# Kernel optimization log

Hardware: AMD Instinct MI355X
Metric: run time of the kernel (lower is better)

## Reference

```python
import jax, jax.numpy as jnp
import numpy as np
from jax import lax

RES = 100      # resolution (default)
BETA = 0.1     # smooth_clamp beta

def smooth_clamp(x, lo, hi):
    return lo + (hi - lo) * jax.nn.sigmoid(BETA * (x - (lo + hi) / 2))

def setup_inputs() -> dict:
    R, C, TQ, TN = 4096, 2048, 4096, 4096
    key = jax.random.key(0)
    k1, k2, k3, k4 = jax.random.split(key, 4)
    t_init = jnp.linspace(0.0, 10.0, TN).astype(jnp.float32)
    t = jnp.sort(jax.random.uniform(k1, (TQ,), jnp.float32, 0.0, 10.0))
    init_conc = jax.random.uniform(k2, (C,), jnp.float32, 0.05, 1.0)
    # sparse stoichiometry: per reaction 2 reactants (-1) and 2 products (+1), distinct compounds
    rng = np.random.default_rng(0)
    idx = np.argsort(rng.random((R, C)), axis=1)[:, :4]
    nu_np = np.zeros((R, C), np.float32)
    nu_np[np.arange(R)[:, None], idx] = np.array([-1.0, -1.0, 1.0, 1.0], np.float32)
    nu = jnp.asarray(nu_np)
    # replicate torch __init__ order/ub math to pick sane raw params f, r
    stoi_f = jnp.where(nu < 0, 0.0, nu)
    stoi_r = jnp.where(nu > 0, 0.0, nu)
    order = jnp.stack([stoi_f.sum(1), -stoi_r.sum(1)], axis=1)          # (R,2)
    ub = TN * 10.0 / jnp.max(jnp.diff(t_init)) / init_conc.sum() ** (order - 1.0)
    kf = jax.random.uniform(k3, (R,), jnp.float32, 0.05, 0.5)
    kr = jax.random.uniform(k4, (R,), jnp.float32, 0.05, 0.5)
    # inv_smooth_clamp with min=0: ub/2 + logit(k/ub)/beta
    inv = lambda y, hi: hi / 2 + (jnp.log(y / hi) - jnp.log1p(-y / hi)) / BETA
    f = inv(kf, ub[:, 0])
    r = inv(kr, ub[:, 1])
    return {"t": t, "f": f, "r": r, "stoichiometry": nu,
            "init_conc": init_conc, "t_init": t_init}

def _pow(x, n):
    # torch pow(x, n) = exp(n * log(x)); x is clamped positive upstream
    return jnp.exp(n * jnp.log(x))

def _dCdt(C, nu, k_p, k_m):
    Cs = jnp.clip(C, 1e-8, 1e3)[None, :]                # (1, C)
    logC = jnp.log(Cs)
    fwd = k_p * jnp.prod(jnp.where(nu < 0, jnp.exp(-nu * logC), 1.0), axis=1, keepdims=True)
    rev = k_m * jnp.prod(jnp.where(nu > 0, jnp.exp(nu * logC), 1.0), axis=1, keepdims=True)
    return (nu * (fwd - rev)).sum(0)                    # (C,)

def reference(t, f, r, stoichiometry, init_conc, t_init):
    nu = stoichiometry
    tg = jnp.linspace(t_init.min(), t_init.max(), RES)  # self.t grid
    stoi_f = jnp.where(nu < 0, 0.0, nu)
    stoi_r = jnp.where(nu > 0, 0.0, nu)
    order = jnp.stack([stoi_f.sum(1), -stoi_r.sum(1)], axis=1)
    ub = t_init.shape[0] * 10.0 / jnp.max(jnp.diff(t_init)) / init_conc.sum() ** (order - 1.0)
    k_p = smooth_clamp(f, 0.0, ub[:, 0])[:, None]       # (R,1)
    k_m = smooth_clamp(r, 0.0, ub[:, 1])[:, None]       # (R,1)
    dts = jnp.diff(tg)                                  # (RES-1,) uniform
    # explicit Euler (default integration_method='euler', is_implicit=False)
    def step(C, dt):
        Cn = C + _dCdt(C, nu, k_p, k_m) * dt
        return Cn, Cn
    _, traj = lax.scan(step, init_conc, dts)
    curve = jnp.concatenate([init_conc[None, :], traj], axis=0)   # (RES, C)
    # interpolation: two nearest grid points per query time
    tq = t.reshape(-1, 1)                               # (TQ,1)
    dist = jnp.abs(tg[None, :] - tq)                    # (TQ,RES)
    idx = jnp.argsort(dist, axis=1)
    i1, i2 = idx[:, 0], idx[:, 1]
    t1 = tg[i1][:, None]
    t2 = tg[i2][:, None]
    c1 = curve[i1]
    c2 = curve[i2]
    slope = (c2 - c1) / (t2 - t1)
    return slope * (tq - t1) + c1                       # (TQ, C)
```

## Files before the change

kernel.cpp:

```cpp
#include <hip/hip_runtime.h>
#include <hip/hip_fp16.h>

#define RESN 100
#define BETAC 0.1f
#define CAPW 14

#define LDS_BARRIER() asm volatile("s_waitcnt lgkmcnt(0)\n\ts_barrier" ::: "memory")


__global__ void scalars_kernel(const float* __restrict__ init_conc, int Cn,
                               const float* __restrict__ t_init, int TN,
                               float* __restrict__ ws) {
    __shared__ float red[256];
    int tid = threadIdx.x;

    float s = 0.f;
    for (int i = tid; i < Cn; i += 256) s += init_conc[i];
    red[tid] = s; __syncthreads();
    for (int o = 128; o; o >>= 1) { if (tid < o) red[tid] += red[tid + o]; __syncthreads(); }
    float S = red[0]; __syncthreads();

    float md = -1e30f;
    for (int i = tid; i < TN - 1; i += 256) md = fmaxf(md, t_init[i + 1] - t_init[i]);
    red[tid] = md; __syncthreads();
    for (int o = 128; o; o >>= 1) { if (tid < o) red[tid] = fmaxf(red[tid], red[tid + o]); __syncthreads(); }
    float MD = red[0]; __syncthreads();

    float mn = 1e30f;
    for (int i = tid; i < TN; i += 256) mn = fminf(mn, t_init[i]);
    red[tid] = mn; __syncthreads();
    for (int o = 128; o; o >>= 1) { if (tid < o) red[tid] = fminf(red[tid], red[tid + o]); __syncthreads(); }
    float TMIN = red[0]; __syncthreads();

    float mx = -1e30f;
    for (int i = tid; i < TN; i += 256) mx = fmaxf(mx, t_init[i]);
    red[tid] = mx; __syncthreads();
    for (int o = 128; o; o >>= 1) { if (tid < o) red[tid] = fmaxf(red[tid], red[tid + o]); __syncthreads(); }
    float TMAX = red[0];

    if (tid == 0) { ws[0] = S; ws[1] = MD; ws[2] = TMIN; ws[3] = TMAX; }
}

__global__ void extract_kernel(const float* __restrict__ nu,
                               const float* __restrict__ f,
                               const float* __restrict__ r,
                               int Rn, int Cn, int TN,
                               float* __restrict__ ws) {
    int row = blockIdx.x;
    int tid = threadIdx.x;
    __shared__ int cntn, cntp;
    __shared__ int negi[2], posi[2];
    __shared__ float red[256];
    if (tid == 0) { cntn = 0; cntp = 0; }
    __syncthreads();

    float sp = 0.f, sn = 0.f;
    const float* nr = nu + (size_t)row * Cn;
    for (int c = tid; c < Cn; c += 256) {
        float v = nr[c];
        if (v < 0.f) {
            int p = atomicAdd(&cntn, 1);
            if (p < 2) negi[p] = c;
            sn -= v;
        } else if (v > 0.f) {
            int p = atomicAdd(&cntp, 1);
            if (p < 2) posi[p] = c;
            sp += v;
        }
    }
    red[tid] = sp; __syncthreads();
    for (int o = 128; o; o >>= 1) { if (tid < o) red[tid] += red[tid + o]; __syncthreads(); }
    float order_f = red[0]; __syncthreads();
    red[tid] = sn; __syncthreads();
    for (int o = 128; o; o >>= 1) { if (tid < o) red[tid] += red[tid + o]; __syncthreads(); }
    float order_r = red[0]; __syncthreads();

    if (tid == 0) {
        float S = ws[0], MD = ws[1];
        float base = (float)TN * 10.0f / MD;
        float ub0 = base / powf(S, order_f - 1.0f);
        float ub1 = base / powf(S, order_r - 1.0f);
        float kp = ub0 / (1.0f + expf(-BETAC * (f[row] - 0.5f * ub0)));
        float km = ub1 / (1.0f + expf(-BETAC * (r[row] - 0.5f * ub1)));
        ws[16 + row] = kp;
        ws[16 + Rn + row] = km;
        int* idx = (int*)(ws + 16 + 2 * Rn);
        idx[4 * row + 0] = negi[0];
        idx[4 * row + 1] = negi[1];
        idx[4 * row + 2] = posi[0];
        idx[4 * row + 3] = posi[1];
    }
}

__global__ void __launch_bounds__(1024) integrate_kernel(
    const float* __restrict__ init_conc, int Cn, int Rn,
    const float* __restrict__ ws, float* __restrict__ curve) {
    __shared__ unsigned int slotsW[CAPW * 2048];
    __shared__ float Cls[2048];
    __shared__ int   cnt[2048];

    int tid = threadIdx.x;
    __half* slotsH = (__half*)slotsW;

    const int4*  idx4   = (const int4*)(ws + 16 + 2 * Rn);
    const float* kp_arr = ws + 16;
    const float* km_arr = ws + 16 + Rn;

    float tmin = ws[2], tmax = ws[3];
    float dt = (tmax - tmin) / (float)(RESN - 1);

    int i1[4], i2[4], j1[4], j2[4];
    float kpv[4], kmv[4];
#pragma unroll
    for (int k = 0; k < 4; k++) {
        int rr = tid + k * 1024;
        int4 v = idx4[rr];
        i1[k] = v.x; i2[k] = v.y; j1[k] = v.z; j2[k] = v.w;
        kpv[k] = kp_arr[rr] * dt;
        kmv[k] = km_arr[rr] * dt;
    }

    cnt[tid] = 0; cnt[tid + 1024] = 0;
#pragma unroll
    for (int k = 0; k < CAPW * 2; k++) slotsW[tid + k * 1024] = 0u;
    __syncthreads();

    int h0[4], h1[4], h2a[4], h3[4];
#pragma unroll
    for (int k = 0; k < 4; k++) {
        int c;
        c = atomicAdd(&cnt[i1[k]], 1); c = min(c, CAPW * 2 - 1);
        h0[k]  = (c >> 1) * 4096 + 2 * i1[k] + (c & 1);
        c = atomicAdd(&cnt[i2[k]], 1); c = min(c, CAPW * 2 - 1);
        h1[k]  = (c >> 1) * 4096 + 2 * i2[k] + (c & 1);
        c = atomicAdd(&cnt[j1[k]], 1); c = min(c, CAPW * 2 - 1);
        h2a[k] = (c >> 1) * 4096 + 2 * j1[k] + (c & 1);
        c = atomicAdd(&cnt[j2[k]], 1); c = min(c, CAPW * 2 - 1);
        h3[k]  = (c >> 1) * 4096 + 2 * j2[k] + (c & 1);
    }
    __syncthreads();

    int nw0 = (cnt[tid] + 1) >> 1;        nw0 = min(nw0, CAPW);
    int nw1 = (cnt[tid + 1024] + 1) >> 1; nw1 = min(nw1, CAPW);

    float Creg[2];
#pragma unroll
    for (int k = 0; k < 2; k++) {
        int s = tid + k * 1024;
        float v = init_conc[s];
        Creg[k] = v;
        Cls[s] = fminf(fmaxf(v, 1e-8f), 1000.f);
        curve[s] = v;
    }
    __syncthreads();

    for (int stp = 0; stp < RESN - 1; ++stp) {
#pragma unroll
        for (int k = 0; k < 4; k++) {
            float rv = kpv[k] * Cls[i1[k]] * Cls[i2[k]]
                     - kmv[k] * Cls[j1[k]] * Cls[j2[k]];
            __half hn = __float2half(-rv);
            __half hp = __float2half(rv);
            slotsH[h0[k]]  = hn;
            slotsH[h1[k]]  = hn;
            slotsH[h2a[k]] = hp;
            slotsH[h3[k]]  = hp;
        }
        LDS_BARRIER();

        {
            float acc0 = 0.f, acc1 = 0.f;
            for (int w = 0; w < nw0; ++w) {
                unsigned int u = slotsW[w * 2048 + tid];
                __half2 h2 = *reinterpret_cast<__half2*>(&u);
                float2 f2 = __half22float2(h2);
                acc0 += f2.x + f2.y;
            }
            for (int w = 0; w < nw1; ++w) {
                unsigned int u = slotsW[w * 2048 + tid + 1024];
                __half2 h2 = *reinterpret_cast<__half2*>(&u);
                float2 f2 = __half22float2(h2);
                acc1 += f2.x + f2.y;
            }
            Creg[0] += acc0;
            Creg[1] += acc1;
            Cls[tid]        = fminf(fmaxf(Creg[0], 1e-8f), 1000.f);
            Cls[tid + 1024] = fminf(fmaxf(Creg[1], 1e-8f), 1000.f);
            curve[(size_t)(stp + 1) * 2048 + tid]        = Creg[0];
            curve[(size_t)(stp + 1) * 2048 + tid + 1024] = Creg[1];
        }
        LDS_BARRIER();
    }
}

__global__ void __launch_bounds__(256) interp_kernel(
    const float* __restrict__ t, const float* __restrict__ curve,
    const float* __restrict__ ws, float* __restrict__ out, int Cn) {
    int q = blockIdx.x;
    float tq = t[q];
    float tmin = ws[2], tmax = ws[3];
    float h = (tmax - tmin) / (float)(RESN - 1);
    float u = (tq - tmin) / h;
    int j0 = (int)floorf(u);
    if (j0 < 0) j0 = 0;
    if (j0 > RESN - 2) j0 = RESN - 2;
    float w = u - (float)j0;
    w = fminf(fmaxf(w, 0.f), 1.f);

    const float4* r0 = (const float4*)(curve + (size_t)j0 * Cn);
    const float4* r1 = (const float4*)(curve + (size_t)(j0 + 1) * Cn);
    float4* o = (float4*)(out + (size_t)q * Cn);
    int n4 = Cn >> 2;
    for (int k = threadIdx.x; k < n4; k += 256) {
        float4 a = r0[k], b = r1[k];
        float4 res;
        res.x = a.x + (b.x - a.x) * w;
        res.y = a.y + (b.y - a.y) * w;
        res.z = a.z + (b.z - a.z) * w;
        res.w = a.w + (b.w - a.w) * w;
        o[k] = res;
    }
}

extern "C" void kernel_launch(void* const* d_in, const int* in_sizes, int n_in,
                              void* d_out, int out_size, void* d_ws, size_t ws_size,
                              hipStream_t stream) {
    const float* t         = (const float*)d_in[0];
    const float* f         = (const float*)d_in[1];
    const float* r         = (const float*)d_in[2];
    const float* nu        = (const float*)d_in[3];
    const float* init_conc = (const float*)d_in[4];
    const float* t_init    = (const float*)d_in[5];
    int TQ = in_sizes[0];
    int Rn = in_sizes[1];
    int Cn = in_sizes[4];
    int TN = in_sizes[5];

    float* ws = (float*)d_ws;
    float* curve = ws + 16 + 6 * (size_t)Rn;

    hipLaunchKernelGGL(scalars_kernel, dim3(1), dim3(256), 0, stream,
                       init_conc, Cn, t_init, TN, ws);
    hipLaunchKernelGGL(extract_kernel, dim3(Rn), dim3(256), 0, stream,
                       nu, f, r, Rn, Cn, TN, ws);
    hipLaunchKernelGGL(integrate_kernel, dim3(1), dim3(1024), 0, stream,
                       init_conc, Cn, Rn, ws, curve);
    hipLaunchKernelGGL(interp_kernel, dim3(TQ), dim3(256), 0, stream,
                       t, curve, ws, (float*)d_out, Cn);
}
```

Baseline: 328.6 us.

## Fuse scalar reductions into integrator and widen LDS slot reads to 64-bit

Removes the separate single-block scalars kernel. The init_conc sum and the t_init reductions now run at the start of the integrate kernel, which also computes the clamped rate constants from the per-row orders written by extract. This saves one launch and takes the rate math off extract's single-thread tail. The per-compound half-precision accumulation slots are regrouped into 4-wide uint2 entries, so each Euler step's gather needs half as many LDS loads. In exchange, the single 1024-thread integrate block does more serial setup work.

```diff
diff --git a/kernel.cpp b/kernel.cpp
--- a/kernel.cpp
+++ b/kernel.cpp
@@ -4,47 +4,13 @@
 #define RESN 100
 #define BETAC 0.1f
 #define CAPW 14
+#define CAPD (CAPW / 2)
 
 #define LDS_BARRIER() asm volatile("s_waitcnt lgkmcnt(0)\n\ts_barrier" ::: "memory")
 
 
-__global__ void scalars_kernel(const float* __restrict__ init_conc, int Cn,
-                               const float* __restrict__ t_init, int TN,
-                               float* __restrict__ ws) {
-    __shared__ float red[256];
-    int tid = threadIdx.x;
-
-    float s = 0.f;
-    for (int i = tid; i < Cn; i += 256) s += init_conc[i];
-    red[tid] = s; __syncthreads();
-    for (int o = 128; o; o >>= 1) { if (tid < o) red[tid] += red[tid + o]; __syncthreads(); }
-    float S = red[0]; __syncthreads();
-
-    float md = -1e30f;
-    for (int i = tid; i < TN - 1; i += 256) md = fmaxf(md, t_init[i + 1] - t_init[i]);
-    red[tid] = md; __syncthreads();
-    for (int o = 128; o; o >>= 1) { if (tid < o) red[tid] = fmaxf(red[tid], red[tid + o]); __syncthreads(); }
-    float MD = red[0]; __syncthreads();
-
-    float mn = 1e30f;
-    for (int i = tid; i < TN; i += 256) mn = fminf(mn, t_init[i]);
-    red[tid] = mn; __syncthreads();
-    for (int o = 128; o; o >>= 1) { if (tid < o) red[tid] = fminf(red[tid], red[tid + o]); __syncthreads(); }
-    float TMIN = red[0]; __syncthreads();
-
-    float mx = -1e30f;
-    for (int i = tid; i < TN; i += 256) mx = fmaxf(mx, t_init[i]);
-    red[tid] = mx; __syncthreads();
-    for (int o = 128; o; o >>= 1) { if (tid < o) red[tid] = fmaxf(red[tid], red[tid + o]); __syncthreads(); }
-    float TMAX = red[0];
-
-    if (tid == 0) { ws[0] = S; ws[1] = MD; ws[2] = TMIN; ws[3] = TMAX; }
-}
-
 __global__ void extract_kernel(const float* __restrict__ nu,
-                               const float* __restrict__ f,
-                               const float* __restrict__ r,
-                               int Rn, int Cn, int TN,
+                               int Rn, int Cn,
                                float* __restrict__ ws) {
     int row = blockIdx.x;
     int tid = threadIdx.x;
@@ -76,14 +42,8 @@
     float order_r = red[0]; __syncthreads();
 
     if (tid == 0) {
-        float S = ws[0], MD = ws[1];
-        float base = (float)TN * 10.0f / MD;
-        float ub0 = base / powf(S, order_f - 1.0f);
-        float ub1 = base / powf(S, order_r - 1.0f);
-        float kp = ub0 / (1.0f + expf(-BETAC * (f[row] - 0.5f * ub0)));
-        float km = ub1 / (1.0f + expf(-BETAC * (r[row] - 0.5f * ub1)));
-        ws[16 + row] = kp;
-        ws[16 + Rn + row] = km;
+        ws[16 + row] = order_f;
+        ws[16 + Rn + row] = order_r;
         int* idx = (int*)(ws + 16 + 2 * Rn);
         idx[4 * row + 0] = negi[0];
         idx[4 * row + 1] = negi[1];
@@ -93,21 +53,54 @@
 }
 
 __global__ void __launch_bounds__(1024) integrate_kernel(
-    const float* __restrict__ init_conc, int Cn, int Rn,
-    const float* __restrict__ ws, float* __restrict__ curve) {
-    __shared__ unsigned int slotsW[CAPW * 2048];
+    const float* __restrict__ init_conc,
+    const float* __restrict__ t_init, int TN,
+    const float* __restrict__ f, const float* __restrict__ r,
+    int Cn, int Rn,
+    float* __restrict__ ws, float* __restrict__ curve) {
+    __shared__ __align__(16) uint2 slotsD[CAPD * 2048];
     __shared__ float Cls[2048];
     __shared__ int   cnt[2048];
 
     int tid = threadIdx.x;
-    __half* slotsH = (__half*)slotsW;
-
-    const int4*  idx4   = (const int4*)(ws + 16 + 2 * Rn);
-    const float* kp_arr = ws + 16;
-    const float* km_arr = ws + 16 + Rn;
-
-    float tmin = ws[2], tmax = ws[3];
-    float dt = (tmax - tmin) / (float)(RESN - 1);
+    __half* slotsH = (__half*)slotsD;
+
+    Cls[tid] = init_conc[tid] + init_conc[tid + 1024];
+    __syncthreads();
+    for (int o = 512; o; o >>= 1) { if (tid < o) Cls[tid] += Cls[tid + o]; __syncthreads(); }
+    float S = Cls[0]; __syncthreads();
+    {
+        float md = -1e30f;
+        for (int i = tid; i < TN - 1; i += 1024) md = fmaxf(md, t_init[i + 1] - t_init[i]);
+        Cls[tid] = md;
+    }
+    __syncthreads();
+    for (int o = 512; o; o >>= 1) { if (tid < o) Cls[tid] = fmaxf(Cls[tid], Cls[tid + o]); __syncthreads(); }
+    float MD = Cls[0]; __syncthreads();
+    {
+        float mn = 1e30f;
+        for (int i = tid; i < TN; i += 1024) mn = fminf(mn, t_init[i]);
+        Cls[tid] = mn;
+    }
+    __syncthreads();
+    for (int o = 512; o; o >>= 1) { if (tid < o) Cls[tid] = fminf(Cls[tid], Cls[tid + o]); __syncthreads(); }
+    float TMIN = Cls[0]; __syncthreads();
+    {
+        float mx = -1e30f;
+        for (int i = tid; i < TN; i += 1024) mx = fmaxf(mx, t_init[i]);
+        Cls[tid] = mx;
+    }
+    __syncthreads();
+    for (int o = 512; o; o >>= 1) { if (tid < o) Cls[tid] = fmaxf(Cls[tid], Cls[tid + o]); __syncthreads(); }
+    float TMAX = Cls[0]; __syncthreads();
+
+    if (tid == 0) { ws[2] = TMIN; ws[3] = TMAX; }
+
+    float dt = (TMAX - TMIN) / (float)(RESN - 1);
+
+    const int4* idx4 = (const int4*)(ws + 16 + 2 * Rn);
+    float logS = logf(S);
+    float base = (float)TN * 10.0f / MD;
 
     int i1[4], i2[4], j1[4], j2[4];
     float kpv[4], kmv[4];
@@ -116,13 +109,17 @@
         int rr = tid + k * 1024;
         int4 v = idx4[rr];
         i1[k] = v.x; i2[k] = v.y; j1[k] = v.z; j2[k] = v.w;
-        kpv[k] = kp_arr[rr] * dt;
-        kmv[k] = km_arr[rr] * dt;
+        float ordf = ws[16 + rr];
+        float ordr = ws[16 + Rn + rr];
+        float ub0 = base * expf(-(ordf - 1.0f) * logS);
+        float ub1 = base * expf(-(ordr - 1.0f) * logS);
+        kpv[k] = dt * ub0 / (1.0f + expf(-BETAC * (f[rr] - 0.5f * ub0)));
+        kmv[k] = dt * ub1 / (1.0f + expf(-BETAC * (r[rr] - 0.5f * ub1)));
     }
 
     cnt[tid] = 0; cnt[tid + 1024] = 0;
 #pragma unroll
-    for (int k = 0; k < CAPW * 2; k++) slotsW[tid + k * 1024] = 0u;
+    for (int k = 0; k < CAPD * 2; k++) slotsD[tid + k * 1024] = make_uint2(0u, 0u);
     __syncthreads();
 
     int h0[4], h1[4], h2a[4], h3[4];
@@ -130,18 +127,18 @@
     for (int k = 0; k < 4; k++) {
         int c;
         c = atomicAdd(&cnt[i1[k]], 1); c = min(c, CAPW * 2 - 1);
-        h0[k]  = (c >> 1) * 4096 + 2 * i1[k] + (c & 1);
+        h0[k]  = (c >> 2) * 8192 + 4 * i1[k] + (c & 3);
         c = atomicAdd(&cnt[i2[k]], 1); c = min(c, CAPW * 2 - 1);
-        h1[k]  = (c >> 1) * 4096 + 2 * i2[k] + (c & 1);
+        h1[k]  = (c >> 2) * 8192 + 4 * i2[k] + (c & 3);
         c = atomicAdd(&cnt[j1[k]], 1); c = min(c, CAPW * 2 - 1);
-        h2a[k] = (c >> 1) * 4096 + 2 * j1[k] + (c & 1);
+        h2a[k] = (c >> 2) * 8192 + 4 * j1[k] + (c & 3);
         c = atomicAdd(&cnt[j2[k]], 1); c = min(c, CAPW * 2 - 1);
-        h3[k]  = (c >> 1) * 4096 + 2 * j2[k] + (c & 1);
-    }
-    __syncthreads();
-
-    int nw0 = (cnt[tid] + 1) >> 1;        nw0 = min(nw0, CAPW);
-    int nw1 = (cnt[tid + 1024] + 1) >> 1; nw1 = min(nw1, CAPW);
+        h3[k]  = (c >> 2) * 8192 + 4 * j2[k] + (c & 3);
+    }
+    __syncthreads();
+
+    int nl0 = min((cnt[tid] + 3) >> 2, CAPD);
+    int nl1 = min((cnt[tid + 1024] + 3) >> 2, CAPD);
 
     float Creg[2];
 #pragma unroll
@@ -170,17 +167,17 @@
 
         {
             float acc0 = 0.f, acc1 = 0.f;
-            for (int w = 0; w < nw0; ++w) {
-                unsigned int u = slotsW[w * 2048 + tid];
-                __half2 h2 = *reinterpret_cast<__half2*>(&u);
-                float2 f2 = __half22float2(h2);
-                acc0 += f2.x + f2.y;
+            for (int l = 0; l < nl0; ++l) {
+                uint2 u = slotsD[l * 2048 + tid];
+                float2 fa = __half22float2(*reinterpret_cast<__half2*>(&u.x));
+                float2 fb = __half22float2(*reinterpret_cast<__half2*>(&u.y));
+                acc0 += (fa.x + fa.y) + (fb.x + fb.y);
             }
-            for (int w = 0; w < nw1; ++w) {
-                unsigned int u = slotsW[w * 2048 + tid + 1024];
-                __half2 h2 = *reinterpret_cast<__half2*>(&u);
-                float2 f2 = __half22float2(h2);
-                acc1 += f2.x + f2.y;
+            for (int l = 0; l < nl1; ++l) {
+                uint2 u = slotsD[l * 2048 + tid + 1024];
+                float2 fa = __half22float2(*reinterpret_cast<__half2*>(&u.x));
+                float2 fb = __half22float2(*reinterpret_cast<__half2*>(&u.y));
+                acc1 += (fa.x + fa.y) + (fb.x + fb.y);
             }
             Creg[0] += acc0;
             Creg[1] += acc1;
@@ -239,12 +236,10 @@
     float* ws = (float*)d_ws;
     float* curve = ws + 16 + 6 * (size_t)Rn;
 
-    hipLaunchKernelGGL(scalars_kernel, dim3(1), dim3(256), 0, stream,
-                       init_conc, Cn, t_init, TN, ws);
     hipLaunchKernelGGL(extract_kernel, dim3(Rn), dim3(256), 0, stream,
-                       nu, f, r, Rn, Cn, TN, ws);
+                       nu, Rn, Cn, ws);
     hipLaunchKernelGGL(integrate_kernel, dim3(1), dim3(1024), 0, stream,
-                       init_conc, Cn, Rn, ws, curve);
+                       init_conc, t_init, TN, f, r, Cn, Rn, ws, curve);
     hipLaunchKernelGGL(interp_kernel, dim3(TQ), dim3(256), 0, stream,
                        t, curve, ws, (float*)d_out, Cn);
 }
```

New measurement: 269.2 us (median of 2 runs). 18.1% less time.
